# Performance work log

Measured on AMD Instinct MI355X. Metric: run time of the kernel, lower is better.

## Reference

```python
import jax, jax.numpy as jnp
import numpy as np

B, N, C_IN, C_EMB, G = 16, 1024, 16, 64, 128
NEG = -1e12


def _lap(m):
    # m @ D^-1/2, transpose, @ D^-1/2  (matches torch code incl. transpose)
    d = jnp.sum(m, axis=1) ** -0.5
    return (m * d[None, :]).T * d[None, :]


def setup_inputs():
    key = jax.random.key(0)
    ks = jax.random.split(key, 16)
    f = jax.random.normal
    return {
        'x': f(ks[0], (B, C_IN, N), jnp.float32),
        'ct': f(ks[1], (B, C_EMB, N), jnp.float32),
        'graph_data': jax.random.uniform(ks[2], (2, N, N), dtype=jnp.float32),
        'emb_w': f(ks[3], (C_EMB, C_IN)) / np.sqrt(C_IN).astype(np.float32),
        'emb_b': f(ks[4], (C_EMB,)) * 0.01,
        'emb2_w': f(ks[5], (N, N)) / np.sqrt(N).astype(np.float32),
        'emb2_b': f(ks[6], (N,)) * 0.01,
        'att_W': f(ks[7], (C_EMB, C_EMB)) / np.sqrt(C_EMB).astype(np.float32),
        'att_a': f(ks[8], (2 * C_EMB, 1)) / np.sqrt(2 * C_EMB).astype(np.float32),
        'att_GL': f(ks[9], (N, G)) / np.sqrt(G).astype(np.float32),
        'uai_w': f(ks[10], (C_EMB, C_EMB)) / np.sqrt(C_EMB).astype(np.float32),
        'uai_b': f(ks[11], (C_EMB,)) * 0.01,
        'lin1_w': f(ks[12], (C_EMB, C_EMB)) / np.sqrt(C_EMB).astype(np.float32),
        'lin2_w': f(ks[13], (C_EMB, C_EMB)) / np.sqrt(C_EMB).astype(np.float32),
        'lin2_b': f(ks[14], (C_EMB,)) * 0.01,
        'ln_w': jnp.ones((C_EMB, N), jnp.float32),
        'ln_b': jnp.zeros((C_EMB, N), jnp.float32),
    }


def reference(x, ct, graph_data, emb_w, emb_b, emb2_w, emb2_b, att_W, att_a,
              att_GL, uai_w, uai_b, lin1_w, lin2_w, lin2_b, ln_w, ln_b):
    # emb: Conv1d k=1 -> leaky_relu -> Linear over node axis N
    h0 = jax.nn.leaky_relu(jnp.einsum('bcn,ec->ben', x, emb_w) + emb_b[None, :, None])
    h0 = jnp.einsum('ben,mn->bem', h0, emb2_w) + emb2_b[None, None, :]
    inp = jnp.swapaxes(h0, 1, 2)  # [B,N,C']

    # InterpositionAttention (repeat/cat factorized: e_ij = leakyrelu(a1.h_i + a2.h_j))
    eye = jnp.eye(N, dtype=x.dtype)
    adj_att = jax.nn.softmax(jax.nn.relu(att_GL @ att_GL.T), axis=-1) + eye
    h = inp @ att_W  # [B,N,C']
    e = jax.nn.leaky_relu((h @ att_a[:C_EMB]) + jnp.swapaxes(h @ att_a[C_EMB:], 1, 2))  # [B,N,N]
    att = jax.nn.softmax(jnp.where(adj_att > 0, e, NEG), axis=2)
    x_att = jnp.swapaxes(jax.nn.relu(att @ h), 1, 2)  # [B,C',N]

    # UAI module (eval mode: dropout off -> all MC samples equal -> sigma = 0)
    mu = jnp.swapaxes(x_att, 1, 2) @ uai_w.T + uai_b  # [B,N,C']
    x_uai = jnp.swapaxes(mu, 1, 2)  # [B,C',N]

    g1 = _lap(graph_data[0] + eye)
    g2 = _lap(graph_data[1] + eye)

    # learned adjacency from pairwise squared distances (cdist p=2, squared)
    xf = jnp.swapaxes(x_uai, 1, 2)  # [B,N,C']
    sq = jnp.sum(xf * xf, axis=-1)
    d2 = jnp.maximum(sq[:, :, None] + sq[:, None, :] - 2.0 * (xf @ jnp.swapaxes(xf, 1, 2)), 0.0)
    gl = jax.nn.softmax(jnp.exp(-d2 / (2.0 * C_EMB)) + eye, axis=-1)  # sigma^2 = emb_size

    def ln(z):  # LayerNorm over last two dims [C', N]
        m = jnp.mean(z, axis=(1, 2), keepdims=True)
        v = jnp.var(z, axis=(1, 2), keepdims=True)
        return (z - m) / jnp.sqrt(v + 1e-5) * ln_w + ln_b

    l1 = lambda z: jnp.einsum('oc,bcn->bon', lin1_w, z)
    l2 = lambda z: jnp.einsum('oc,bcn->bon', lin2_w, z) + lin2_b[None, :, None]

    x_new = ln(l1(x_uai) @ gl + l1(l1(x_uai) @ g1) @ g2)
    ft = jax.nn.gelu(ln(l2(x_uai) @ gl + l2(l2(x_uai) @ g1) @ g2), approximate=False)
    rt = ft  # rt is computed by the identical expression (dropout off)

    ct_new = ft * ct + x_new - ft * x_new
    ht = rt * jax.nn.elu(ct_new) + x_uai - rt * x_uai
    return (ht, ct_new)
```

## Files before the change

kernel.cpp:

```cpp
#include <hip/hip_runtime.h>
#include <math.h>

typedef unsigned short u16;
typedef __attribute__((ext_vector_type(8))) short short8;
typedef __attribute__((ext_vector_type(4))) float floatx4;

constexpr int BATCH = 16;
constexpr int NI = 1024;
constexpr int CE = 64;
constexpr int CI = 16;
constexpr long long NN2  = (long long)NI * NI;
constexpr long long BCN  = (long long)BATCH * CE * NI;
constexpr long long BNv  = (long long)BATCH * NI;
constexpr long long BNN  = (long long)BATCH * NI * NI;
constexpr long long S1 = (long long)CE * NI;
constexpr long long S2 = 2 * S1;

__device__ __forceinline__ float lrelu01(float x) { return x > 0.f ? x : 0.01f * x; }

__device__ __forceinline__ u16 f2bf(float f) {
  unsigned u = __builtin_bit_cast(unsigned, f);
  return (u16)((u + 0x7fffu + ((u >> 16) & 1u)) >> 16);
}
__device__ __forceinline__ float bf2f(u16 h) {
  unsigned u = ((unsigned)h) << 16;
  return __builtin_bit_cast(float, u);
}
__device__ __forceinline__ unsigned fkey(float f) {
  unsigned u = __builtin_bit_cast(unsigned, f);
  return (u & 0x80000000u) ? ~u : (u | 0x80000000u);
}
__device__ __forceinline__ float funkey(unsigned k) {
  unsigned u = (k & 0x80000000u) ? (k & 0x7fffffffu) : ~k;
  return __builtin_bit_cast(float, u);
}

template<int BM, int BN, int MODE>
__global__ __launch_bounds__(256) void mgemm(
    const u16* __restrict__ Ag, const u16* __restrict__ B1g, const u16* __restrict__ B2g,
    int K1, int K, int lda, int ldb, long long bsA, long long bsB1,
    float* __restrict__ Cf, u16* __restrict__ Cb, int ldc, long long bsC,
    const float* __restrict__ aux1, const float* __restrict__ aux2,
    const float* __restrict__ aux3, const float* __restrict__ aux4,
    float* __restrict__ Zout)
{
  constexpr int RM = BM / 2, RN = BN / 2, MI = RM / 16, NJ = RN / 16;
  __shared__ __align__(16) u16 As[BM * 64];
  __shared__ __align__(16) u16 Bs[BN * 64];
  const int z = blockIdx.z;
  const int n0 = blockIdx.x * BN;
  const int r0 = blockIdx.y * BM;
  const u16* Ab = Ag + (long long)z * bsA + (long long)r0 * lda;
  const u16* Bb1 = B1g + (long long)z * bsB1 + (long long)n0 * ldb;
  const int tid = threadIdx.x;
  const int lane = tid & 63;
  const int wid = tid >> 6;
  const int wr = wid >> 1, wc = wid & 1;
  const int q = lane >> 4, mlow = lane & 15;

  floatx4 acc[MI][NJ] = {};
  float zp[(BM * 8) / 256] = {};

  for (int k0 = 0; k0 < K; k0 += 64) {
    if constexpr (MODE == 10) {
      const float* s1z = aux2 + (long long)z * NI;
      const float* s2z = aux3 + (long long)z * NI;
      const float mb = funkey(((const unsigned*)Zout)[z]);
#pragma unroll
      for (int s = 0; s < (BM * 8) / 256; s++) {
        int cid = tid + s * 256;
        int r = cid >> 3, craw = cid & 7;
        float s1r = s1z[r0 + r];
        float mr = lrelu01(s1r + mb);
        const float* sp = s2z + k0 + craw * 8;
        float4 sa = *(const float4*)sp;
        float4 sb = *(const float4*)(sp + 4);
        float p0 = __expf(lrelu01(s1r + sa.x) - mr);
        float p1 = __expf(lrelu01(s1r + sa.y) - mr);
        float p2 = __expf(lrelu01(s1r + sa.z) - mr);
        float p3 = __expf(lrelu01(s1r + sa.w) - mr);
        float p4 = __expf(lrelu01(s1r + sb.x) - mr);
        float p5 = __expf(lrelu01(s1r + sb.y) - mr);
        float p6 = __expf(lrelu01(s1r + sb.z) - mr);
        float p7 = __expf(lrelu01(s1r + sb.w) - mr);
        zp[s] += p0 + p1 + p2 + p3 + p4 + p5 + p6 + p7;
        uint4 v;
        v.x = (unsigned)f2bf(p0) | ((unsigned)f2bf(p1) << 16);
        v.y = (unsigned)f2bf(p2) | ((unsigned)f2bf(p3) << 16);
        v.z = (unsigned)f2bf(p4) | ((unsigned)f2bf(p5) << 16);
        v.w = (unsigned)f2bf(p6) | ((unsigned)f2bf(p7) << 16);
        *(uint4*)&As[(r * 8 + (craw ^ (r & 7))) * 8] = v;
      }
    } else {
      const u16* Asrc = Ab + k0;
#pragma unroll
      for (int s = 0; s < (BM * 8) / 256; s++) {
        int cid = tid + s * 256;
        int r = cid >> 3, craw = cid & 7;
        uint4 v = *(const uint4*)(Asrc + (long long)r * lda + craw * 8);
        *(uint4*)&As[(r * 8 + (craw ^ (r & 7))) * 8] = v;
      }
    }
    {
      const u16* Bsrc = (k0 < K1) ? (Bb1 + k0)
                                  : (B2g + (long long)n0 * ldb + (k0 - K1));
#pragma unroll
      for (int s = 0; s < (BN * 8) / 256; s++) {
        int cid = tid + s * 256;
        int r = cid >> 3, craw = cid & 7;
        uint4 v = *(const uint4*)(Bsrc + (long long)r * ldb + craw * 8);
        *(uint4*)&Bs[(r * 8 + (craw ^ (r & 7))) * 8] = v;
      }
    }
    __syncthreads();
#pragma unroll
    for (int kh = 0; kh < 2; kh++) {
      const int kc = kh * 4 + q;
      short8 afr[MI], bfr[NJ];
#pragma unroll
      for (int i = 0; i < MI; i++) {
        int row = wr * RM + i * 16 + mlow;
        afr[i] = *(const short8*)&As[(row * 8 + (kc ^ (row & 7))) * 8];
      }
#pragma unroll
      for (int j = 0; j < NJ; j++) {
        int row = wc * RN + j * 16 + mlow;
        bfr[j] = *(const short8*)&Bs[(row * 8 + (kc ^ (row & 7))) * 8];
      }
#pragma unroll
      for (int i = 0; i < MI; i++)
#pragma unroll
        for (int j = 0; j < NJ; j++)
          acc[i][j] = __builtin_amdgcn_mfma_f32_16x16x32_bf16(afr[i], bfr[j], acc[i][j], 0, 0, 0);
    }
    __syncthreads();
  }

  if constexpr (MODE == 3) {
    const float* sqb = aux1 + (long long)z * NI;
#pragma unroll
    for (int i = 0; i < MI; i++) {
#pragma unroll
      for (int rg = 0; rg < 4; rg++) {
        int r = r0 + wr * RM + i * 16 + q * 4 + rg;
        float sqi = sqb[r];
        float rsum = 0.f;
#pragma unroll
        for (int j = 0; j < NJ; j++) {
          int ncol = n0 + wc * RN + j * 16 + mlow;
          float d2 = fmaxf(sqi + sqb[ncol] - 2.f * acc[i][j][rg], 0.f);
          float w = __expf(__expf(-d2 * (1.f / 128.f)) + (r == ncol ? 1.f : 0.f) - 2.f);
          Cb[(long long)z * bsC + (long long)r * ldc + ncol] = f2bf(w);
          rsum += w;
        }
        rsum += __shfl_xor(rsum, 1);
        rsum += __shfl_xor(rsum, 2);
        rsum += __shfl_xor(rsum, 4);
        rsum += __shfl_xor(rsum, 8);
        if (mlow == 0) atomicAdd(&Zout[(long long)z * NI + r], rsum);
      }
    }
  } else if constexpr (MODE == 2) {
#pragma unroll
    for (int i = 0; i < MI; i++) {
#pragma unroll
      for (int rg = 0; rg < 4; rg++) {
        int r = r0 + wr * RM + i * 16 + q * 4 + rg;
        float sqp = 0.f;
#pragma unroll
        for (int j = 0; j < NJ; j++) {
          int ncol = n0 + wc * RN + j * 16 + mlow;
          float v = acc[i][j][rg] + aux1[ncol];
          Cb[(long long)z * bsC + (long long)r * ldc + ncol] = f2bf(v);
          sqp = fmaf(v, v, sqp);
        }
        sqp += __shfl_xor(sqp, 1);
        sqp += __shfl_xor(sqp, 2);
        sqp += __shfl_xor(sqp, 4);
        sqp += __shfl_xor(sqp, 8);
        if (mlow == 0) atomicAdd(&Zout[(long long)z * NI + r], sqp);
      }
    }
  } else if constexpr (MODE == 11) {
    float* sred = (float*)As;
#pragma unroll
    for (int i = 0; i < MI; i++) {
#pragma unroll
      for (int rg = 0; rg < 4; rg++) {
        int rloc = wr * RM + i * 16 + q * 4 + rg;
        int r = r0 + rloc;
        float rb = aux3[r];
        float ps1 = 0.f, ps2 = 0.f;
#pragma unroll
        for (int j = 0; j < NJ; j++) {
          int ncol = n0 + wc * RN + j * 16 + mlow;
          float v = acc[i][j][rg] + rb;
          Cb[(long long)z * bsC + (long long)r * ldc + ncol] = f2bf(v);
          ps1 = fmaf(v, aux1[ncol], ps1);
          ps2 = fmaf(v, aux2[ncol], ps2);
        }
        ps1 += __shfl_xor(ps1, 1); ps1 += __shfl_xor(ps1, 2);
        ps1 += __shfl_xor(ps1, 4); ps1 += __shfl_xor(ps1, 8);
        ps2 += __shfl_xor(ps2, 1); ps2 += __shfl_xor(ps2, 2);
        ps2 += __shfl_xor(ps2, 4); ps2 += __shfl_xor(ps2, 8);
        if (mlow == 0) { sred[rloc * 2 + wc] = ps1; sred[128 + rloc * 2 + wc] = ps2; }
      }
    }
    __syncthreads();
    if (tid < 64) {
      float v1 = sred[tid * 2] + sred[tid * 2 + 1];
      float v2 = sred[128 + tid * 2] + sred[128 + tid * 2 + 1];
      Cf[(long long)z * NI + r0 + tid] = v1;
      Zout[(long long)z * NI + r0 + tid] = v2;
      float mx = v2;
      for (int off = 1; off < 64; off <<= 1) mx = fmaxf(mx, __shfl_xor(mx, off));
      if (tid == 0) atomicMax((unsigned*)B2g + z, fkey(mx));
    }
  } else if constexpr (MODE == 10) {
    float* zred = (float*)As;
    float* zinv = (float*)As + 512;
#pragma unroll
    for (int s = 0; s < 2; s++)
      zred[((tid >> 3) + s * 32) * 8 + (tid & 7)] = zp[s];
    __syncthreads();
    if (tid < 64) {
      float sum = 0.f;
#pragma unroll
      for (int j = 0; j < 8; j++) sum += zred[tid * 8 + j];
      zinv[tid] = 1.f / sum;
    }
    __syncthreads();
#pragma unroll
    for (int i = 0; i < MI; i++) {
#pragma unroll
      for (int j = 0; j < NJ; j++) {
#pragma unroll
        for (int rg = 0; rg < 4; rg++) {
          int rloc = wr * RM + i * 16 + q * 4 + rg;
          int ncol = n0 + wc * RN + j * 16 + mlow;
          float v = acc[i][j][rg] * zinv[rloc];
          v = fmaxf(v, 0.f);
          Cb[(long long)z * bsC + (long long)(r0 + rloc) * ldc + ncol] = f2bf(v);
        }
      }
    }
  } else if constexpr (MODE == 5) {
    float ts = 0.f, tss = 0.f;
#pragma unroll
    for (int i = 0; i < MI; i++) {
#pragma unroll
      for (int j = 0; j < NJ; j++) {
#pragma unroll
        for (int rg = 0; rg < 4; rg++) {
          int r = r0 + wr * RM + i * 16 + q * 4 + rg;
          int ncol = n0 + wc * RN + j * 16 + mlow;
          float v = acc[i][j][rg];
          v += aux3[r] * aux1[(long long)z * NI + ncol] + aux4[r] * aux2[ncol];
          Cf[(long long)z * bsC + (long long)r * ldc + ncol] = v;
          ts += v;
          tss = fmaf(v, v, tss);
        }
      }
    }
    float* red = (float*)As;
    red[tid] = ts; red[256 + tid] = tss;
    __syncthreads();
    for (int st = 128; st > 0; st >>= 1) {
      if (tid < st) { red[tid] += red[tid + st]; red[256 + tid] += red[256 + tid + st]; }
      __syncthreads();
    }
    if (tid == 0) {
      const int half = r0 >> 6;
      atomicAdd(&Zout[z * 2 + half], red[0]);
      atomicAdd(&Zout[32 + z * 2 + half], red[256]);
    }
  } else {
#pragma unroll
    for (int i = 0; i < MI; i++) {
#pragma unroll
      for (int j = 0; j < NJ; j++) {
#pragma unroll
        for (int rg = 0; rg < 4; rg++) {
          int r = r0 + wr * RM + i * 16 + q * 4 + rg;
          int ncol = n0 + wc * RN + j * 16 + mlow;
          float v = acc[i][j][rg];
          if constexpr (MODE == 4) {
            int blk = r >> 6, oo = r & 63;
            int drow = ((blk & 1) << 6) + oo;
            if (blk < 2) v = v / aux1[(long long)z * NI + ncol];
            Cb[(long long)z * bsC + (long long)drow * 2048 + (long long)(blk >> 1) * 1024 + ncol] =
                f2bf(v);
          } else {
            Cb[(long long)z * bsC + (long long)r * ldc + ncol] = f2bf(v);
          }
        }
      }
    }
  }
}

__global__ __launch_bounds__(256) void lap_rowsum(const float* __restrict__ gd,
                                                  float* __restrict__ dr)
{
  const int ki = blockIdx.x;
  const float* row = gd + (long long)ki * NI;
  float s = 0.f;
  for (int j = threadIdx.x; j < NI; j += 256) s += row[j];
  __shared__ float red[256];
  red[threadIdx.x] = s; __syncthreads();
  for (int st = 128; st > 0; st >>= 1) {
    if (threadIdx.x < st) red[threadIdx.x] += red[threadIdx.x + st];
    __syncthreads();
  }
  if (threadIdx.x == 0) dr[ki] = rsqrtf(red[0] + 1.f);
}

__global__ __launch_bounds__(256) void mega_prep(
    const float* __restrict__ l1w, const float* __restrict__ l2w,
    const float* __restrict__ l2b, const float* __restrict__ uaiw,
    const float* __restrict__ attW, const float* __restrict__ atta,
    u16* __restrict__ stack4, float* __restrict__ rb2ext, float* __restrict__ rl2ext,
    u16* __restrict__ uaiw_bf, u16* __restrict__ attwT_bf, float* __restrict__ w12,
    const float* __restrict__ emb2w, u16* __restrict__ emb2w_bf,
    const float* __restrict__ x, const float* __restrict__ ew,
    const float* __restrict__ eb, u16* __restrict__ h0a,
    const float* __restrict__ gd, const float* __restrict__ dsum,
    u16* __restrict__ g2t, u16* __restrict__ g1,
    float* __restrict__ cs1)
{
  __shared__ float sm[1088];
  const int bid = blockIdx.x;
  const int t = threadIdx.x;
  if (bid < 98) {
    const int gid = bid * 256 + t;
    if (gid < 4096) {
      stack4[gid] = f2bf(l1w[gid]);
    } else if (gid < 8192) {
      stack4[gid] = f2bf(l2w[gid - 4096]);
    } else if (gid < 12288) {
      int tt = gid - 8192, o = tt >> 6, m = tt & 63;
      float s = 0.f;
      for (int c = 0; c < 64; c++) s = fmaf(l1w[o * 64 + c], l1w[c * 64 + m], s);
      stack4[gid] = f2bf(s);
    } else if (gid < 16384) {
      int tt = gid - 12288, o = tt >> 6, m = tt & 63;
      float s = 0.f;
      for (int c = 0; c < 64; c++) s = fmaf(l2w[o * 64 + c], l2w[c * 64 + m], s);
      stack4[gid] = f2bf(s);
    } else if (gid < 16512) {
      int r = gid - 16384;
      rb2ext[r] = (r < 64) ? 0.f : l2b[r - 64];
    } else if (gid < 16640) {
      int r = gid - 16512;
      float v = 0.f;
      if (r >= 64) { int o = r - 64; for (int c = 0; c < 64; c++) v = fmaf(l2w[o * 64 + c], l2b[c], v); }
      rl2ext[r] = v;
    } else if (gid < 20736) {
      uaiw_bf[gid - 16640] = f2bf(uaiw[gid - 16640]);
    } else if (gid < 24832) {
      int idx = gid - 20736;
      int k = idx >> 6, e = idx & 63;
      attwT_bf[idx] = f2bf(attW[e * 64 + k]);
    } else if (gid < 24960) {
      int c = gid - 24832;
      int cc = c & 63, which = c >> 6;
      float s = 0.f;
      for (int k = 0; k < 64; k++) s = fmaf(attW[cc * 64 + k], atta[which * 64 + k], s);
      w12[c] = s;
    }
  } else if (bid < 4194) {
    const long long i = (long long)(bid - 98) * 256 + t;
    emb2w_bf[i] = f2bf(emb2w[i]);
  } else if (bid < 5218) {
    const int be = bid - 4194;
    const int b = be >> 6, e = be & 63;
    float* w = sm;
    if (t < CI) w[t] = ew[e * CI + t];
    __syncthreads();
    const float bias = eb[e];
    const float* xb = x + (long long)b * CI * NI;
    u16* outp = h0a + (long long)be * NI;
    for (int n = t; n < NI; n += 256) {
      float a = bias;
#pragma unroll
      for (int c = 0; c < CI; c++) a = fmaf(xb[c * NI + n], w[c], a);
      outp[n] = f2bf(lrelu01(a));
    }
  } else if (bid < 9314) {
    const long long idx = (long long)(bid - 5218) * 256 + t;
    const int m = (int)(idx >> 10), j = (int)(idx & 1023);
    const float* d = dsum + NI;
    float v = (gd[NN2 + idx] + (m == j ? 1.f : 0.f)) * d[m] * d[j];
    g2t[idx] = f2bf(v);
  } else if (bid < 10338) {
    const int sub = bid - 9314;
    const int bx = (sub & 31) * 32, by = (sub >> 5) * 32;
    const int lx = t & 31, ly = t >> 5;
    float* tile = sm;
    for (int yy = ly; yy < 32; yy += 8)
      tile[yy * 33 + lx] = gd[(long long)(by + yy) * NI + bx + lx];
    __syncthreads();
    for (int yy = ly; yy < 32; yy += 8) {
      const int i = bx + yy, j = by + lx;
      float v = (tile[lx * 33 + yy] + (i == j ? 1.f : 0.f)) * dsum[i] * dsum[j];
      g1[(long long)i * NI + j] = f2bf(v);
    }
  } else {
    const int n = bid - 10338;
    float s = 0.f;
    for (int i = t; i < NI; i += 256) s = fmaf(gd[(long long)n * NI + i], dsum[i], s);
    float* red = sm;
    red[t] = s; __syncthreads();
    for (int st = 128; st > 0; st >>= 1) {
      if (t < st) red[t] += red[t + st];
      __syncthreads();
    }
    if (t == 0) cs1[n] = dsum[n] * (red[0] + dsum[n]);
  }
}

__global__ __launch_bounds__(256) void csv2_kernel(const float* __restrict__ gd1,
                                                   const float* __restrict__ d,
                                                   const float* __restrict__ cs1,
                                                   float* __restrict__ cs2,
                                                   float* __restrict__ v2)
{
  const int m = blockIdx.x;
  float s = 0.f, sv = 0.f;
  for (int n = threadIdx.x; n < NI; n += 256) {
    float g = gd1[(long long)m * NI + n] * d[n];
    s += g;
    sv = fmaf(g, cs1[n], sv);
  }
  __shared__ float r1[256], r2[256];
  r1[threadIdx.x] = s; r2[threadIdx.x] = sv; __syncthreads();
  for (int st = 128; st > 0; st >>= 1) {
    if (threadIdx.x < st) { r1[threadIdx.x] += r1[threadIdx.x + st]; r2[threadIdx.x] += r2[threadIdx.x + st]; }
    __syncthreads();
  }
  if (threadIdx.x == 0) {
    cs2[m] = d[m] * (r1[0] + d[m]);
    v2[m] = d[m] * (r2[0] + d[m] * cs1[m]);
  }
}

__global__ __launch_bounds__(256) void cc_kernel(const u16* __restrict__ W,
                                                 const float* __restrict__ Zgl,
                                                 const float* __restrict__ cs2,
                                                 float* __restrict__ cc)
{
  const int b = blockIdx.y;
  const int wid = threadIdx.x >> 6, lane = threadIdx.x & 63;
  const int m = blockIdx.x * 4 + wid;
  const u16* row = W + (long long)b * NN2 + (long long)m * NI;
  const float* zz = Zgl + (long long)b * NI;
  float s = 0.f;
#pragma unroll
  for (int it = 0; it < 4; it++) {
    const int j0 = it * 256 + lane * 4;
    uint2 pk = *(const uint2*)(row + j0);
    float4 zv = *(const float4*)(zz + j0);
    s += bf2f((u16)(pk.x & 0xffff)) / zv.x + bf2f((u16)(pk.x >> 16)) / zv.y
       + bf2f((u16)(pk.y & 0xffff)) / zv.z + bf2f((u16)(pk.y >> 16)) / zv.w;
  }
  for (int off = 1; off < 64; off <<= 1) s += __shfl_xor(s, off);
  if (lane == 0) cc[(long long)b * NI + m] = s + cs2[m];
}

__global__ __launch_bounds__(256) void ln_final_t(const float* __restrict__ T,
                                                  const float* __restrict__ stats,
                                                  const float* __restrict__ lnw,
                                                  const float* __restrict__ lnb,
                                                  const float* __restrict__ ct,
                                                  const u16* __restrict__ xuT,
                                                  float* __restrict__ outp)
{
  __shared__ float xs[64 * 65];
  const int blk = blockIdx.x;
  const int b = blk >> 4;
  const int n0 = (blk & 15) << 6;
  const int t = threadIdx.x;
  const int tc = t & 63, tr = t >> 6;
#pragma unroll
  for (int i = 0; i < 16; i++) {
    int nn = i * 4 + tr;
    xs[tc * 65 + nn] = bf2f(xuT[((long long)b << 16) + (long long)(n0 + nn) * 64 + tc]);
  }
  __syncthreads();
  const float inv_n = 1.f / 65536.f;
  const float m0 = stats[b * 2] * inv_n;
  const float m1 = stats[b * 2 + 1] * inv_n;
  const float rs0 = rsqrtf(fmaxf(stats[32 + b * 2] * inv_n - m0 * m0, 0.f) + 1e-5f);
  const float rs1 = rsqrtf(fmaxf(stats[32 + b * 2 + 1] * inv_n - m1 * m1, 0.f) + 1e-5f);
#pragma unroll
  for (int j = 0; j < 16; j++) {
    const int c = j * 4 + tr;
    const int n = n0 + tc;
    const int rem = c * NI + n;
    const long long toff = (long long)b * S2 + rem;
    const float t0 = T[toff];
    const float t1 = T[toff + S1];
    const float w = lnw[rem], bb = lnb[rem];
    const float xn = (t0 - m0) * rs0 * w + bb;
    float ft = (t1 - m1) * rs1 * w + bb;
    ft = 0.5f * ft * (1.f + erff(ft * 0.70710678118654752f));
    const float u = xs[c * 65 + tc];
    const long long oidx = ((long long)b << 16) + rem;
    const float cn = fmaf(ft, ct[oidx] - xn, xn);
    const float el = cn > 0.f ? cn : expm1f(cn);
    outp[oidx] = fmaf(ft, el - u, u);
    outp[BCN + oidx] = cn;
  }
}

extern "C" void kernel_launch(void* const* d_in, const int* in_sizes, int n_in,
                              void* d_out, int out_size, void* d_ws, size_t ws_size,
                              hipStream_t stream)
{
  (void)in_sizes; (void)n_in; (void)out_size; (void)ws_size;
  const float* x      = (const float*)d_in[0];
  const float* ct     = (const float*)d_in[1];
  const float* gdata  = (const float*)d_in[2];
  const float* emb_w  = (const float*)d_in[3];
  const float* emb_b  = (const float*)d_in[4];
  const float* emb2_w = (const float*)d_in[5];
  const float* emb2_b = (const float*)d_in[6];
  const float* att_W  = (const float*)d_in[7];
  const float* att_a  = (const float*)d_in[8];
  const float* uai_w  = (const float*)d_in[10];
  const float* uai_b  = (const float*)d_in[11];
  const float* lin1_w = (const float*)d_in[12];
  const float* lin2_w = (const float*)d_in[13];
  const float* lin2_b = (const float*)d_in[14];
  const float* ln_w   = (const float*)d_in[15];
  const float* ln_b   = (const float*)d_in[16];
  float* outp = (float*)d_out;

  float* ws = (float*)d_ws;
  long long o = 0;
  auto af = [&](long long n) { float* p = ws + o; o += (n + 63) & ~63LL; return p; };
  auto au = [&](long long n) { return (u16*)af((n + 1) / 2); };

  float* Tacc    = af(S2 * BATCH);
  float* s1      = af(BNv);
  float* s2      = af(BNv);
  float* dsum    = af(2 * NI);
  float* cs1v    = af(NI);
  float* cs2v    = af(NI);
  float* v2v     = af(NI);
  float* ccv     = af(BNv);
  float* rb2ext  = af(128);
  float* rl2ext  = af(128);
  float* w12     = af(128);
  float* zeroreg = af(2 * BNv + 80);
  float* Zgl     = zeroreg;
  float* sqv     = zeroreg + BNv;
  float* stats   = zeroreg + 2 * BNv;
  unsigned* s2mU = (unsigned*)(stats + 64);
  u16* emb2w_bf  = au(NN2);
  u16* h0a_bf    = au(S1 * BATCH);
  u16* h0Tb      = au(S1 * BATCH);
  u16* hTb       = au(S1 * BATCH);
  u16* xattb     = au(S1 * BATCH);
  u16* xuaiTb    = au(S1 * BATCH);
  u16* g1b       = au(NN2);
  u16* g2tb      = au(NN2);
  u16* G12b      = au(NN2);
  u16* Abig      = au((long long)BATCH * 128 * 2048);
  u16* stack4    = au(256 * 64);
  u16* uaiw_bf   = au(CE * CE);
  u16* attwT_bf  = au(CE * CE);
  u16* bigW      = au(BNN);

  hipMemsetAsync(zeroreg, 0, (2 * BNv + 80) * sizeof(float), stream);

  lap_rowsum<<<2 * NI, 256, 0, stream>>>(gdata, dsum);

  mega_prep<<<11362, 256, 0, stream>>>(
      lin1_w, lin2_w, lin2_b, uai_w, att_W, att_a,
      stack4, rb2ext, rl2ext, uaiw_bf, attwT_bf, w12,
      emb2_w, emb2w_bf, x, emb_w, emb_b, h0a_bf,
      gdata, dsum, g2tb, g1b, cs1v);

  csv2_kernel<<<NI, 256, 0, stream>>>(gdata + NN2, dsum + NI, cs1v, cs2v, v2v);

  mgemm<64, 64, 6><<<dim3(16, 16, 1), 256, 0, stream>>>(
      g2tb, g1b, nullptr, NI, NI, NI, NI, 0, 0,
      nullptr, G12b, NI, 0, nullptr, nullptr, nullptr, nullptr, nullptr);

  mgemm<64, 64, 11><<<dim3(1, 16, BATCH), 256, 0, stream>>>(
      emb2w_bf, h0a_bf, (const u16*)s2mU, NI, NI, NI, NI, 0, S1,
      s1, h0Tb, CE, S1, w12, w12 + 64, emb2_b, nullptr, s2);

  mgemm<64, 64, 6><<<dim3(16, 1, BATCH), 256, 0, stream>>>(
      attwT_bf, h0Tb, nullptr, CE, CE, CE, CE, 0, S1,
      nullptr, hTb, NI, S1, nullptr, nullptr, nullptr, nullptr, nullptr);

  mgemm<64, 64, 10><<<dim3(1, 16, BATCH), 256, 0, stream>>>(
      hTb, hTb, nullptr, NI, NI, NI, NI, 0, S1,
      nullptr, xattb, CE, S1, nullptr, s1, s2, nullptr, (float*)s2mU);

  mgemm<64, 64, 2><<<dim3(1, 16, BATCH), 256, 0, stream>>>(
      xattb, uaiw_bf, nullptr, CE, CE, CE, CE, S1, 0,
      nullptr, xuaiTb, CE, S1, uai_b, nullptr, nullptr, nullptr, sqv);

  mgemm<128, 128, 3><<<dim3(8, 8, BATCH), 256, 0, stream>>>(
      xuaiTb, xuaiTb, nullptr, CE, CE, CE, CE, S1, S1,
      nullptr, bigW, NI, NN2, sqv, nullptr, nullptr, nullptr, Zgl);

  cc_kernel<<<dim3(NI / 4, BATCH), 256, 0, stream>>>(bigW, Zgl, cs2v, ccv);

  mgemm<64, 64, 4><<<dim3(16, 4, BATCH), 256, 0, stream>>>(
      stack4, xuaiTb, nullptr, CE, CE, CE, CE, 0, S1,
      nullptr, Abig, 0, (long long)128 * 2048, Zgl, nullptr, nullptr, nullptr, nullptr);

  mgemm<64, 64, 5><<<dim3(16, 2, BATCH), 256, 0, stream>>>(
      Abig, bigW, G12b, NI, 2 * NI, 2048, NI, (long long)128 * 2048, NN2,
      Tacc, nullptr, NI, S2, ccv, v2v, rb2ext, rl2ext, stats);

  ln_final_t<<<256, 256, 0, stream>>>(Tacc, stats, ln_w, ln_b, ct, xuaiTb, outp);
}
```

Before: 262.8 us.

## Fuse attention aggregation GEMM with UAI linear projection in one kernel

Merges the attention-weighted aggregation (old mode 10) and the following 64x64 UAI linear layer with row squared-norm accumulation (old mode 2) into a new mode 13. The intermediate x_att tile stays in shared memory and is multiplied by the uai weight with MFMA, so the xattb global buffer round trip and one kernel launch go away. The row tile also shrinks from 64 to 32 rows, doubling the grid to add parallelism, at the cost of more redundant softmax exp work per block and extra LDS and synchronisation.

```diff
diff --git a/kernel.cpp b/kernel.cpp
--- a/kernel.cpp
+++ b/kernel.cpp
@@ -47,6 +47,7 @@
   constexpr int RM = BM / 2, RN = BN / 2, MI = RM / 16, NJ = RN / 16;
   __shared__ __align__(16) u16 As[BM * 64];
   __shared__ __align__(16) u16 Bs[BN * 64];
+  __shared__ __align__(16) u16 xa[MODE == 13 ? 32 * 72 : 1];
   const int z = blockIdx.z;
   const int n0 = blockIdx.x * BN;
   const int r0 = blockIdx.y * BM;
@@ -62,10 +63,10 @@
   float zp[(BM * 8) / 256] = {};
 
   for (int k0 = 0; k0 < K; k0 += 64) {
-    if constexpr (MODE == 10) {
+    if constexpr (MODE == 13) {
       const float* s1z = aux2 + (long long)z * NI;
       const float* s2z = aux3 + (long long)z * NI;
-      const float mb = funkey(((const unsigned*)Zout)[z]);
+      const float mb = funkey(((const unsigned*)aux4)[z]);
 #pragma unroll
       for (int s = 0; s < (BM * 8) / 256; s++) {
         int cid = tid + s * 256;
@@ -160,27 +161,6 @@
         if (mlow == 0) atomicAdd(&Zout[(long long)z * NI + r], rsum);
       }
     }
-  } else if constexpr (MODE == 2) {
-#pragma unroll
-    for (int i = 0; i < MI; i++) {
-#pragma unroll
-      for (int rg = 0; rg < 4; rg++) {
-        int r = r0 + wr * RM + i * 16 + q * 4 + rg;
-        float sqp = 0.f;
-#pragma unroll
-        for (int j = 0; j < NJ; j++) {
-          int ncol = n0 + wc * RN + j * 16 + mlow;
-          float v = acc[i][j][rg] + aux1[ncol];
-          Cb[(long long)z * bsC + (long long)r * ldc + ncol] = f2bf(v);
-          sqp = fmaf(v, v, sqp);
-        }
-        sqp += __shfl_xor(sqp, 1);
-        sqp += __shfl_xor(sqp, 2);
-        sqp += __shfl_xor(sqp, 4);
-        sqp += __shfl_xor(sqp, 8);
-        if (mlow == 0) atomicAdd(&Zout[(long long)z * NI + r], sqp);
-      }
-    }
   } else if constexpr (MODE == 11) {
     float* sred = (float*)As;
 #pragma unroll
@@ -216,33 +196,68 @@
       for (int off = 1; off < 64; off <<= 1) mx = fmaxf(mx, __shfl_xor(mx, off));
       if (tid == 0) atomicMax((unsigned*)B2g + z, fkey(mx));
     }
-  } else if constexpr (MODE == 10) {
-    float* zred = (float*)As;
-    float* zinv = (float*)As + 512;
-#pragma unroll
-    for (int s = 0; s < 2; s++)
-      zred[((tid >> 3) + s * 32) * 8 + (tid & 7)] = zp[s];
-    __syncthreads();
-    if (tid < 64) {
+  } else if constexpr (MODE == 13) {
+    float* zred = (float*)xa;
+    float* zinv = (float*)xa + 256;
+    zred[(tid >> 3) * 8 + (tid & 7)] = zp[0];
+    __syncthreads();
+    if (tid < 32) {
       float sum = 0.f;
 #pragma unroll
       for (int j = 0; j < 8; j++) sum += zred[tid * 8 + j];
       zinv[tid] = 1.f / sum;
     }
     __syncthreads();
-#pragma unroll
-    for (int i = 0; i < MI; i++) {
-#pragma unroll
-      for (int j = 0; j < NJ; j++) {
-#pragma unroll
-        for (int rg = 0; rg < 4; rg++) {
-          int rloc = wr * RM + i * 16 + q * 4 + rg;
-          int ncol = n0 + wc * RN + j * 16 + mlow;
-          float v = acc[i][j][rg] * zinv[rloc];
-          v = fmaxf(v, 0.f);
-          Cb[(long long)z * bsC + (long long)(r0 + rloc) * ldc + ncol] = f2bf(v);
-        }
-      }
+    float zr[4];
+#pragma unroll
+    for (int rg = 0; rg < 4; rg++) zr[rg] = zinv[wr * 16 + q * 4 + rg];
+    __syncthreads();
+#pragma unroll
+    for (int j = 0; j < NJ; j++) {
+#pragma unroll
+      for (int rg = 0; rg < 4; rg++) {
+        int row = wr * 16 + q * 4 + rg;
+        int col = wc * RN + j * 16 + mlow;
+        float v = fmaxf(acc[0][j][rg] * zr[rg], 0.f);
+        xa[row * 72 + col] = f2bf(v);
+      }
+    }
+#pragma unroll
+    for (int s = 0; s < 2; s++) {
+      int cid = tid + s * 256;
+      int r = cid >> 3, craw = cid & 7;
+      *(uint4*)&Bs[(r * 8 + (craw ^ (r & 7))) * 8] =
+          *(const uint4*)(B2g + r * 64 + craw * 8);
+    }
+    __syncthreads();
+    floatx4 acc2[2] = {};
+#pragma unroll
+    for (int kh = 0; kh < 2; kh++) {
+      const int kc = kh * 4 + q;
+      short8 a2 = *(const short8*)&xa[(wr * 16 + mlow) * 72 + kc * 8];
+#pragma unroll
+      for (int j = 0; j < 2; j++) {
+        int orow = wc * 32 + j * 16 + mlow;
+        short8 b2 = *(const short8*)&Bs[(orow * 8 + (kc ^ (orow & 7))) * 8];
+        acc2[j] = __builtin_amdgcn_mfma_f32_16x16x32_bf16(a2, b2, acc2[j], 0, 0, 0);
+      }
+    }
+#pragma unroll
+    for (int rg = 0; rg < 4; rg++) {
+      int row = r0 + wr * 16 + q * 4 + rg;
+      float sqp = 0.f;
+#pragma unroll
+      for (int j = 0; j < 2; j++) {
+        int o = wc * 32 + j * 16 + mlow;
+        float v = acc2[j][rg] + aux1[o];
+        Cb[(long long)z * bsC + (long long)row * ldc + o] = f2bf(v);
+        sqp = fmaf(v, v, sqp);
+      }
+      sqp += __shfl_xor(sqp, 1);
+      sqp += __shfl_xor(sqp, 2);
+      sqp += __shfl_xor(sqp, 4);
+      sqp += __shfl_xor(sqp, 8);
+      if (mlow == 0) atomicAdd(&Zout[(long long)z * NI + row], sqp);
     }
   } else if constexpr (MODE == 5) {
     float ts = 0.f, tss = 0.f;
@@ -561,7 +576,6 @@
   u16* h0a_bf    = au(S1 * BATCH);
   u16* h0Tb      = au(S1 * BATCH);
   u16* hTb       = au(S1 * BATCH);
-  u16* xattb     = au(S1 * BATCH);
   u16* xuaiTb    = au(S1 * BATCH);
   u16* g1b       = au(NN2);
   u16* g2tb      = au(NN2);
@@ -596,13 +610,9 @@
       attwT_bf, h0Tb, nullptr, CE, CE, CE, CE, 0, S1,
       nullptr, hTb, NI, S1, nullptr, nullptr, nullptr, nullptr, nullptr);
 
-  mgemm<64, 64, 10><<<dim3(1, 16, BATCH), 256, 0, stream>>>(
-      hTb, hTb, nullptr, NI, NI, NI, NI, 0, S1,
-      nullptr, xattb, CE, S1, nullptr, s1, s2, nullptr, (float*)s2mU);
-
-  mgemm<64, 64, 2><<<dim3(1, 16, BATCH), 256, 0, stream>>>(
-      xattb, uaiw_bf, nullptr, CE, CE, CE, CE, S1, 0,
-      nullptr, xuaiTb, CE, S1, uai_b, nullptr, nullptr, nullptr, sqv);
+  mgemm<32, 64, 13><<<dim3(1, 32, BATCH), 256, 0, stream>>>(
+      hTb, hTb, uaiw_bf, NI, NI, NI, NI, 0, S1,
+      nullptr, xuaiTb, CE, S1, uai_b, s1, s2, (const float*)s2mU, sqv);
 
   mgemm<128, 128, 3><<<dim3(8, 8, BATCH), 256, 0, stream>>>(
       xuaiTb, xuaiTb, nullptr, CE, CE, CE, CE, S1, S1,
```

Measured after the change: 257.2 us. 2.1% less time.
